# Kernel optimization log

Hardware: AMD Instinct MI355X
Metric: run time of the kernel (lower is better)

Reference implementation:

```python
import math
import jax, jax.numpy as jnp
import numpy as np

B, S, H, NH = 2, 2048, 1024, 16
HD = H // NH


def setup_inputs() -> dict:
    key = jax.random.key(0)
    k1, k2, k3 = jax.random.split(key, 3)
    scale = 1.0 / math.sqrt(H)
    return {
        "hidden_states": jax.random.normal(k1, (B, S, H), dtype=jnp.float32),
        "attention_mask": jnp.ones((B, 1, S, S), dtype=jnp.float32),
        "qkv_w": jax.random.normal(k2, (3 * H, H), dtype=jnp.float32) * scale,
        "qkv_b": jnp.zeros((3 * H,), dtype=jnp.float32),
        "dense_w": jax.random.normal(k3, (H, H), dtype=jnp.float32) * scale,
        "dense_b": jnp.zeros((H,), dtype=jnp.float32),
    }


def reference(hidden_states, attention_mask, qkv_w, qkv_b, dense_w, dense_b):
    # qkv projection: torch Linear y = x @ W^T + b
    mixed = hidden_states @ qkv_w.T + qkv_b            # [B,S,3H]
    mixed = mixed.reshape(B, S, NH, 3 * HD).transpose(0, 2, 1, 3)  # [B,NH,S,3HD]
    q, k, v = jnp.split(mixed, 3, axis=-1)             # each [B,NH,S,HD]
    scores = jnp.einsum("bhqd,bhkd->bhqk", q, k) / math.sqrt(HD)
    scores = scores * attention_mask - 10000.0 * (1.0 - attention_mask)
    probs = jax.nn.softmax(scores, axis=-1)            # dropout p=0 -> identity
    ctx = jnp.einsum("bhqk,bhkd->bhqd", probs, v)      # [B,NH,S,HD]
    ctx = ctx.transpose(0, 2, 1, 3).reshape(B, S, H)
    out = ctx @ dense_w.T + dense_b                    # output dropout p=0
    return out
```

## Files before the change

kernel.cpp:

```cpp
#include <hip/hip_runtime.h>
#include <hip/hip_bf16.h>
#include <stdint.h>

#define BB 2
#define SS 2048
#define HH 1024
#define NHH 16
#define HDD 64
#define MM (BB*SS)
#define N1 (3*HH)
#define NT (SS/64)
#define LOG2E 1.44269504f

using bf16 = __hip_bfloat16;
typedef __attribute__((ext_vector_type(8))) short bf16x8;
typedef __attribute__((ext_vector_type(4))) float f32x4;

__device__ inline unsigned short f2bfu(float f) {
  union { bf16 h; unsigned short u; } c;
  c.h = __float2bfloat16(f);
  return c.u;
}

__device__ inline unsigned int cvtpk(float lo, float hi) {
  unsigned int r;
  asm("v_cvt_pk_bf16_f32 %0, %1, %2" : "=v"(r) : "v"(lo), "v"(hi));
  return r;
}

__device__ inline void load_lds16(const void* g, void* l) {
  __builtin_amdgcn_global_load_lds(
      (const __attribute__((address_space(1))) void*)g,
      (__attribute__((address_space(3))) void*)l, 16, 0, 0);
}

__device__ inline f32x4 mfma16(bf16x8 a, bf16x8 b, f32x4 c) {
  return __builtin_amdgcn_mfma_f32_16x16x32_bf16(a, b, c, 0, 0, 0);
}

__global__ __launch_bounds__(256) void cvt_f32_bf16(const float* __restrict__ in,
                                                    unsigned short* __restrict__ out,
                                                    int n4) {
  int i = blockIdx.x * blockDim.x + threadIdx.x;
  int st = gridDim.x * blockDim.x;
  for (; i < n4; i += st) {
    float4 v = reinterpret_cast<const float4*>(in)[i];
    ushort4 o;
    o.x = f2bfu(v.x); o.y = f2bfu(v.y); o.z = f2bfu(v.z); o.w = f2bfu(v.w);
    reinterpret_cast<ushort4*>(out)[i] = o;
  }
}

__global__ __launch_bounds__(256) void mask_flags_kernel(const float* __restrict__ mask,
                                                         unsigned char* __restrict__ flags) {
  int t = blockIdx.x;
  int b = t >> 10, qt = (t >> 5) & 31, kt = t & 31;
  const float* mb = mask + ((size_t)b * SS + qt * 64) * SS + kt * 64;
  int row = threadIdx.x >> 2, c0 = (threadIdx.x & 3) * 16;
  int ok = 1;
#pragma unroll
  for (int j = 0; j < 4; ++j) {
    float4 v = *reinterpret_cast<const float4*>(mb + (size_t)row * SS + c0 + j * 4);
    ok &= (v.x == 1.f) & (v.y == 1.f) & (v.z == 1.f) & (v.w == 1.f);
  }
  ok = __all(ok);
  __shared__ int s[4];
  if ((threadIdx.x & 63) == 0) s[threadIdx.x >> 6] = ok;
  __syncthreads();
  if (threadIdx.x == 0) flags[t] = (unsigned char)(s[0] & s[1] & s[2] & s[3]);
}

__global__ __launch_bounds__(256) void vtrans_kernel(const unsigned short* __restrict__ mixed,
                                                     unsigned short* __restrict__ vT) {
  __shared__ unsigned short t[64 * 72];
  const int st = blockIdx.x, bh = blockIdx.y;
  const int b = bh >> 4, h = bh & 15;
  const int r = threadIdx.x >> 2, c0 = (threadIdx.x & 3) * 16;

  const unsigned short* src = mixed + ((size_t)(b * SS) + st * 64) * N1 + h * 192 + 128;
  union { bf16x8 v; unsigned short u[8]; } A, B;
  A.v = *reinterpret_cast<const bf16x8*>(src + (size_t)r * N1 + c0);
  B.v = *reinterpret_cast<const bf16x8*>(src + (size_t)r * N1 + c0 + 8);
#pragma unroll
  for (int j = 0; j < 8; ++j) t[(c0 + j) * 72 + r] = A.u[j];
#pragma unroll
  for (int j = 0; j < 8; ++j) t[(c0 + 8 + j) * 72 + r] = B.u[j];
  __syncthreads();

  unsigned short* dst = vT + ((size_t)bh * HDD + r) * SS + st * 64 + c0;
  bf16x8 o0 = *reinterpret_cast<const bf16x8*>(&t[r * 72 + c0]);
  bf16x8 o1 = *reinterpret_cast<const bf16x8*>(&t[r * 72 + c0 + 8]);
  *reinterpret_cast<bf16x8*>(dst) = o0;
  *reinterpret_cast<bf16x8*>(dst + 8) = o1;
}

template <bool OUT_BF16>
__global__ __launch_bounds__(256) void gemm_bt(const unsigned short* __restrict__ A,
                                               const unsigned short* __restrict__ Bt,
                                               const float* __restrict__ bias,
                                               void* __restrict__ Cv,
                                               int Ndim, int Kdim) {
  __shared__ __align__(16) unsigned short As[128 * 32];
  __shared__ __align__(16) unsigned short Bs[128 * 32];

  const int tid = threadIdx.x;
  const int wave = tid >> 6, lane = tid & 63;
  const int m0 = blockIdx.x * 128;
  const int n0 = blockIdx.y * 128;
  const int wm = (wave >> 1) * 64, wn = (wave & 1) * 64;
  const int lrow = lane & 15;
  const int lk8 = (lane >> 4) * 8;
  const int r4 = (lane >> 4) * 4;

  f32x4 acc[4][4];
  const f32x4 z = {0.f, 0.f, 0.f, 0.f};
  for (int i = 0; i < 4; ++i)
    for (int j = 0; j < 4; ++j) acc[i][j] = z;

  for (int k0 = 0; k0 < Kdim; k0 += 32) {
#pragma unroll
    for (int it = 0; it < 2; ++it) {
      int idx = it * 256 + tid;
      int row = idx >> 2, seg = idx & 3;
      load_lds16(A + (size_t)(m0 + row) * Kdim + k0 + seg * 8, &As[row * 32 + seg * 8]);
      load_lds16(Bt + (size_t)(n0 + row) * Kdim + k0 + seg * 8, &Bs[row * 32 + seg * 8]);
    }
    __syncthreads();

    bf16x8 af[4], bfr[4];
#pragma unroll
    for (int i = 0; i < 4; ++i)
      af[i] = *reinterpret_cast<const bf16x8*>(&As[(wm + i * 16 + lrow) * 32 + lk8]);
#pragma unroll
    for (int j = 0; j < 4; ++j)
      bfr[j] = *reinterpret_cast<const bf16x8*>(&Bs[(wn + j * 16 + lrow) * 32 + lk8]);
#pragma unroll
    for (int i = 0; i < 4; ++i)
#pragma unroll
      for (int j = 0; j < 4; ++j)
        acc[i][j] = mfma16(af[i], bfr[j], acc[i][j]);
    __syncthreads();
  }

#pragma unroll
  for (int i = 0; i < 4; ++i) {
#pragma unroll
    for (int j = 0; j < 4; ++j) {
      int col = n0 + wn + j * 16 + lrow;
      float bv = bias[col];
#pragma unroll
      for (int r = 0; r < 4; ++r) {
        int row = m0 + wm + i * 16 + r4 + r;
        float v = acc[i][j][r] + bv;
        if (OUT_BF16) {
          ((unsigned short*)Cv)[(size_t)row * Ndim + col] = f2bfu(v);
        } else {
          ((float*)Cv)[(size_t)row * Ndim + col] = v;
        }
      }
    }
  }
}

__global__ __launch_bounds__(256, 4) void attn_kernel(const unsigned short* __restrict__ mixed,
                                                      const unsigned short* __restrict__ vT,
                                                      const float* __restrict__ mask,
                                                      const unsigned char* __restrict__ flags,
                                                      unsigned short* __restrict__ ctx) {
  __shared__ __align__(16) unsigned short Ks[2][64 * 64];
  __shared__ __align__(16) unsigned short Vt[2][64 * 64];
  __shared__ __align__(16) unsigned short QP[64 * 64];

  const int tid = threadIdx.x, wave = tid >> 6, lane = tid & 63;
  const int ql = lane & 15;
  const int g = lane >> 4;
  const int q0 = blockIdx.x * 64;
  const int bh = blockIdx.y;
  const int b = bh / NHH, hh = bh % NHH;

  const unsigned short* qbase = mixed + (size_t)(b * SS) * N1 + hh * 192;
  const unsigned short* kbase = qbase + 64;
  const unsigned short* vtbase = vT + ((size_t)(b * NHH + hh) * HDD) * SS;
  const float* mbase = mask + (size_t)b * SS * SS;
  const unsigned char* fl = flags + ((size_t)b * 32 + blockIdx.x) * 32;

  const int srow = tid >> 3, sseg = tid & 7;
  const int swst = (sseg ^ (srow & 7)) << 3;

  load_lds16(qbase + (size_t)(q0 + srow) * N1 + swst, &QP[srow * 64 + sseg * 8]);
  load_lds16(qbase + (size_t)(q0 + 32 + srow) * N1 + swst, &QP[(32 + srow) * 64 + sseg * 8]);
  load_lds16(kbase + (size_t)srow * N1 + swst, &Ks[0][srow * 64 + sseg * 8]);
  load_lds16(kbase + (size_t)(32 + srow) * N1 + swst, &Ks[0][(32 + srow) * 64 + sseg * 8]);
  load_lds16(vtbase + (size_t)srow * SS + swst, &Vt[0][srow * 64 + sseg * 8]);
  load_lds16(vtbase + (size_t)(32 + srow) * SS + swst, &Vt[0][(32 + srow) * 64 + sseg * 8]);
  __syncthreads();

  const int qrow = wave * 16 + ql;
  const bf16x8 qf0 = *reinterpret_cast<const bf16x8*>(
      &QP[qrow * 64 + ((g ^ (qrow & 7)) << 3)]);
  const bf16x8 qf1 = *reinterpret_cast<const bf16x8*>(
      &QP[qrow * 64 + (((g + 4) ^ (qrow & 7)) << 3)]);
  __syncthreads();

  const int s0 = (g ^ (ql & 7)) << 3;
  const int s1 = ((g + 4) ^ (ql & 7)) << 3;
  const unsigned short* KrA = &Ks[0][ql * 64 + s0];
  const unsigned short* KrB = &Ks[0][ql * 64 + s1];
  const unsigned short* VrA = &Vt[0][ql * 64 + s0];
  const unsigned short* VrB = &Vt[0][ql * 64 + s1];
  unsigned short* Ps = &QP[wave * 1024];
  const int X = (ql & 7) << 3;
  unsigned short* Pw0 = &Ps[ql * 64 + ((4 * g) ^ X)];
  unsigned short* Pw1 = &Ps[ql * 64 + ((16 + 4 * g) ^ X)];
  unsigned short* Pw2 = &Ps[ql * 64 + ((32 + 4 * g) ^ X)];
  unsigned short* Pw3 = &Ps[ql * 64 + ((48 + 4 * g) ^ X)];
  const unsigned short* Pr0 = &Ps[ql * 64 + ((8 * g) ^ X)];
  const unsigned short* Pr1 = &Ps[ql * 64 + ((32 + 8 * g) ^ X)];

  const unsigned short* kpre = kbase + (size_t)(64 + srow) * N1 + swst;
  const unsigned short* vpre = vtbase + (size_t)srow * SS + 64 + swst;

  f32x4 oacc[4];
  const f32x4 z = {0.f, 0.f, 0.f, 0.f};
  for (int fd = 0; fd < 4; ++fd) oacc[fd] = z;
  float lsum = 0.f;
  const float C2 = 0.125f * LOG2E;

#define TILE_BODY(CUR_, KT_, HAVENEXT_)                                         \
  {                                                                             \
    const int kt_ = (KT_);                                                      \
    if (HAVENEXT_) {                                                            \
      load_lds16(kpre, &Ks[(CUR_)^1][srow * 64 + sseg * 8]);                    \
      load_lds16(kpre + 32 * N1, &Ks[(CUR_)^1][(32 + srow) * 64 + sseg * 8]);   \
      load_lds16(vpre, &Vt[(CUR_)^1][srow * 64 + sseg * 8]);                    \
      load_lds16(vpre + 32 * SS, &Vt[(CUR_)^1][(32 + srow) * 64 + sseg * 8]);   \
    }                                                                           \
    kpre += 64 * N1; vpre += 64;                                                \
    f32x4 sacc[4];                                                              \
    __builtin_amdgcn_s_setprio(1);                                              \
    _Pragma("unroll")                                                           \
    for (int n = 0; n < 4; ++n) {                                               \
      bf16x8 k0 = *reinterpret_cast<const bf16x8*>(KrA + (CUR_)*4096 + n*1024); \
      bf16x8 k1 = *reinterpret_cast<const bf16x8*>(KrB + (CUR_)*4096 + n*1024); \
      sacc[n] = mfma16(k0, qf0, z);                                             \
      sacc[n] = mfma16(k1, qf1, sacc[n]);                                       \
    }                                                                           \
    __builtin_amdgcn_s_setprio(0);                                              \
    const bool allones = fl[kt_] != 0;                                          \
    float pv[4][4];                                                             \
    if (allones) {                                                              \
      _Pragma("unroll")                                                         \
      for (int n = 0; n < 4; ++n)                                               \
        _Pragma("unroll")                                                       \
        for (int r = 0; r < 4; ++r)                                             \
          pv[n][r] = exp2f(sacc[n][r] * C2);                                    \
    } else {                                                                    \
      int qq = q0 + wave * 16 + ql;                                             \
      _Pragma("unroll")                                                         \
      for (int n = 0; n < 4; ++n)                                               \
        _Pragma("unroll")                                                       \
        for (int r = 0; r < 4; ++r) {                                           \
          int kk = kt_ * 64 + 16 * n + 4 * g + r;                               \
          float mv = mbase[(size_t)qq * SS + kk];                               \
          float s = sacc[n][r] * 0.125f;                                        \
          pv[n][r] = exp2f((s * mv - 10000.f * (1.f - mv)) * LOG2E);            \
        }                                                                       \
    }                                                                           \
    {                                                                           \
      float t00 = (pv[0][0] + pv[0][1]) + (pv[0][2] + pv[0][3]);                \
      float t01 = (pv[1][0] + pv[1][1]) + (pv[1][2] + pv[1][3]);                \
      float t10 = (pv[2][0] + pv[2][1]) + (pv[2][2] + pv[2][3]);                \
      float t11 = (pv[3][0] + pv[3][1]) + (pv[3][2] + pv[3][3]);                \
      lsum += (t00 + t01) + (t10 + t11);                                        \
    }                                                                           \
    { uint2 w; w.x = cvtpk(pv[0][0], pv[0][1]); w.y = cvtpk(pv[0][2], pv[0][3]);\
      *reinterpret_cast<uint2*>(Pw0) = w; }                                     \
    { uint2 w; w.x = cvtpk(pv[1][0], pv[1][1]); w.y = cvtpk(pv[1][2], pv[1][3]);\
      *reinterpret_cast<uint2*>(Pw1) = w; }                                     \
    { uint2 w; w.x = cvtpk(pv[2][0], pv[2][1]); w.y = cvtpk(pv[2][2], pv[2][3]);\
      *reinterpret_cast<uint2*>(Pw2) = w; }                                     \
    { uint2 w; w.x = cvtpk(pv[3][0], pv[3][1]); w.y = cvtpk(pv[3][2], pv[3][3]);\
      *reinterpret_cast<uint2*>(Pw3) = w; }                                     \
    bf16x8 pa0 = *reinterpret_cast<const bf16x8*>(Pr0);                         \
    bf16x8 pa1 = *reinterpret_cast<const bf16x8*>(Pr1);                         \
    __builtin_amdgcn_s_setprio(1);                                              \
    _Pragma("unroll")                                                           \
    for (int fd = 0; fd < 4; ++fd) {                                            \
      bf16x8 bv0 = *reinterpret_cast<const bf16x8*>(VrA + (CUR_)*4096 + fd*1024);\
      bf16x8 bv1 = *reinterpret_cast<const bf16x8*>(VrB + (CUR_)*4096 + fd*1024);\
      oacc[fd] = mfma16(pa0, bv0, oacc[fd]);                                    \
      oacc[fd] = mfma16(pa1, bv1, oacc[fd]);                                    \
    }                                                                           \
    __builtin_amdgcn_s_setprio(0);                                              \
    __syncthreads();                                                            \
  }

  for (int kt = 0; kt < NT; kt += 2) {
    TILE_BODY(0, kt, true)
    TILE_BODY(1, kt + 1, (kt + 2 < NT))
  }
#undef TILE_BODY

  float lrun = lsum;
  lrun += __shfl_xor(lrun, 16, 64);
  lrun += __shfl_xor(lrun, 32, 64);
  float invl = 1.f / lrun;
#pragma unroll
  for (int r = 0; r < 4; ++r) {
    float inv = __shfl(invl, g * 4 + r, 64);
    int qq = q0 + wave * 16 + g * 4 + r;
    unsigned short* cp = ctx + (size_t)(b * SS + qq) * HH + hh * HDD;
#pragma unroll
    for (int fd = 0; fd < 4; ++fd)
      cp[fd * 16 + ql] = f2bfu(oacc[fd][r] * inv);
  }
}

extern "C" void kernel_launch(void* const* d_in, const int* in_sizes, int n_in,
                              void* d_out, int out_size, void* d_ws, size_t ws_size,
                              hipStream_t stream) {
  const float* hs      = (const float*)d_in[0];
  const float* mask    = (const float*)d_in[1];
  const float* qkv_w   = (const float*)d_in[2];
  const float* qkv_b   = (const float*)d_in[3];
  const float* dense_w = (const float*)d_in[4];
  const float* dense_b = (const float*)d_in[5];
  float* out = (float*)d_out;

  char* ws = (char*)d_ws;
  unsigned short* hs_b     = (unsigned short*)(ws);
  unsigned short* qkvw_b   = (unsigned short*)(ws + 8388608);
  unsigned short* densew_b = (unsigned short*)(ws + 14680064);
  unsigned short* mixed_b  = (unsigned short*)(ws + 16777216);
  unsigned short* ctx_b    = (unsigned short*)(ws + 41943040);
  unsigned char*  flags    = (unsigned char*)(ws + 50331648);
  unsigned short* vT_b     = (unsigned short*)(ws + 50335744);

  cvt_f32_bf16<<<2048, 256, 0, stream>>>(hs, hs_b, (MM * HH) / 4);
  cvt_f32_bf16<<<2048, 256, 0, stream>>>(qkv_w, qkvw_b, (N1 * HH) / 4);
  cvt_f32_bf16<<<1024, 256, 0, stream>>>(dense_w, densew_b, (HH * HH) / 4);
  mask_flags_kernel<<<BB * 32 * 32, 256, 0, stream>>>(mask, flags);

  gemm_bt<true><<<dim3(MM / 128, N1 / 128), 256, 0, stream>>>(
      hs_b, qkvw_b, qkv_b, mixed_b, N1, HH);

  vtrans_kernel<<<dim3(SS / 64, BB * NHH), 256, 0, stream>>>(mixed_b, vT_b);

  attn_kernel<<<dim3(SS / 64, BB * NHH), 256, 0, stream>>>(
      mixed_b, vT_b, mask, flags, ctx_b);

  gemm_bt<false><<<dim3(MM / 128, HH / 128), 256, 0, stream>>>(
      ctx_b, densew_b, dense_b, out, HH, HH);
}
```

Before: 157.2 us.

## Load V tiles directly into registers instead of staging through LDS

V^T fragments for the PV MFMA are now loaded from global memory straight into per-lane registers, double-buffered across key tiles, and the LDS Vt buffers are removed. This is meant to cut LDS traffic and LDS footprint, which could allow more occupancy. In exchange each wave issues its own global loads for V, so V is fetched redundantly across the four waves, and register pressure rises by 16 bf16x8 vectors, which may reduce occupancy under the 256x4 launch bounds.

```diff
diff --git a/kernel.cpp b/kernel.cpp
--- a/kernel.cpp
+++ b/kernel.cpp
@@ -168,7 +168,6 @@
                                                       const unsigned char* __restrict__ flags,
                                                       unsigned short* __restrict__ ctx) {
   __shared__ __align__(16) unsigned short Ks[2][64 * 64];
-  __shared__ __align__(16) unsigned short Vt[2][64 * 64];
   __shared__ __align__(16) unsigned short QP[64 * 64];
 
   const int tid = threadIdx.x, wave = tid >> 6, lane = tid & 63;
@@ -191,8 +190,22 @@
   load_lds16(qbase + (size_t)(q0 + 32 + srow) * N1 + swst, &QP[(32 + srow) * 64 + sseg * 8]);
   load_lds16(kbase + (size_t)srow * N1 + swst, &Ks[0][srow * 64 + sseg * 8]);
   load_lds16(kbase + (size_t)(32 + srow) * N1 + swst, &Ks[0][(32 + srow) * 64 + sseg * 8]);
-  load_lds16(vtbase + (size_t)srow * SS + swst, &Vt[0][srow * 64 + sseg * 8]);
-  load_lds16(vtbase + (size_t)(32 + srow) * SS + swst, &Vt[0][(32 + srow) * 64 + sseg * 8]);
+
+  const unsigned short* vp0 = vtbase + (size_t)(0 * 16 + ql) * SS + g * 8;
+  const unsigned short* vp1 = vtbase + (size_t)(1 * 16 + ql) * SS + g * 8;
+  const unsigned short* vp2 = vtbase + (size_t)(2 * 16 + ql) * SS + g * 8;
+  const unsigned short* vp3 = vtbase + (size_t)(3 * 16 + ql) * SS + g * 8;
+
+  bf16x8 vrA[8], vrB[8];
+  vrA[0] = *reinterpret_cast<const bf16x8*>(vp0);
+  vrA[1] = *reinterpret_cast<const bf16x8*>(vp1);
+  vrA[2] = *reinterpret_cast<const bf16x8*>(vp2);
+  vrA[3] = *reinterpret_cast<const bf16x8*>(vp3);
+  vrA[4] = *reinterpret_cast<const bf16x8*>(vp0 + 32);
+  vrA[5] = *reinterpret_cast<const bf16x8*>(vp1 + 32);
+  vrA[6] = *reinterpret_cast<const bf16x8*>(vp2 + 32);
+  vrA[7] = *reinterpret_cast<const bf16x8*>(vp3 + 32);
+  vp0 += 64; vp1 += 64; vp2 += 64; vp3 += 64;
   __syncthreads();
 
   const int qrow = wave * 16 + ql;
@@ -206,8 +219,6 @@
   const int s1 = ((g + 4) ^ (ql & 7)) << 3;
   const unsigned short* KrA = &Ks[0][ql * 64 + s0];
   const unsigned short* KrB = &Ks[0][ql * 64 + s1];
-  const unsigned short* VrA = &Vt[0][ql * 64 + s0];
-  const unsigned short* VrB = &Vt[0][ql * 64 + s1];
   unsigned short* Ps = &QP[wave * 1024];
   const int X = (ql & 7) << 3;
   unsigned short* Pw0 = &Ps[ql * 64 + ((4 * g) ^ X)];
@@ -218,7 +229,6 @@
   const unsigned short* Pr1 = &Ps[ql * 64 + ((32 + 8 * g) ^ X)];
 
   const unsigned short* kpre = kbase + (size_t)(64 + srow) * N1 + swst;
-  const unsigned short* vpre = vtbase + (size_t)srow * SS + 64 + swst;
 
   f32x4 oacc[4];
   const f32x4 z = {0.f, 0.f, 0.f, 0.f};
@@ -226,16 +236,23 @@
   float lsum = 0.f;
   const float C2 = 0.125f * LOG2E;
 
-#define TILE_BODY(CUR_, KT_, HAVENEXT_)                                         \
+#define TILE_BODY(CUR_, KT_, HAVENEXT_, VCUR, VNXT)                             \
   {                                                                             \
     const int kt_ = (KT_);                                                      \
     if (HAVENEXT_) {                                                            \
       load_lds16(kpre, &Ks[(CUR_)^1][srow * 64 + sseg * 8]);                    \
       load_lds16(kpre + 32 * N1, &Ks[(CUR_)^1][(32 + srow) * 64 + sseg * 8]);   \
-      load_lds16(vpre, &Vt[(CUR_)^1][srow * 64 + sseg * 8]);                    \
-      load_lds16(vpre + 32 * SS, &Vt[(CUR_)^1][(32 + srow) * 64 + sseg * 8]);   \
-    }                                                                           \
-    kpre += 64 * N1; vpre += 64;                                                \
+      VNXT[0] = *reinterpret_cast<const bf16x8*>(vp0);                          \
+      VNXT[1] = *reinterpret_cast<const bf16x8*>(vp1);                          \
+      VNXT[2] = *reinterpret_cast<const bf16x8*>(vp2);                          \
+      VNXT[3] = *reinterpret_cast<const bf16x8*>(vp3);                          \
+      VNXT[4] = *reinterpret_cast<const bf16x8*>(vp0 + 32);                     \
+      VNXT[5] = *reinterpret_cast<const bf16x8*>(vp1 + 32);                     \
+      VNXT[6] = *reinterpret_cast<const bf16x8*>(vp2 + 32);                     \
+      VNXT[7] = *reinterpret_cast<const bf16x8*>(vp3 + 32);                     \
+    }                                                                           \
+    kpre += 64 * N1;                                                            \
+    vp0 += 64; vp1 += 64; vp2 += 64; vp3 += 64;                                 \
     f32x4 sacc[4];                                                              \
     __builtin_amdgcn_s_setprio(1);                                              \
     _Pragma("unroll")                                                           \
@@ -286,18 +303,16 @@
     __builtin_amdgcn_s_setprio(1);                                              \
     _Pragma("unroll")                                                           \
     for (int fd = 0; fd < 4; ++fd) {                                            \
-      bf16x8 bv0 = *reinterpret_cast<const bf16x8*>(VrA + (CUR_)*4096 + fd*1024);\
-      bf16x8 bv1 = *reinterpret_cast<const bf16x8*>(VrB + (CUR_)*4096 + fd*1024);\
-      oacc[fd] = mfma16(pa0, bv0, oacc[fd]);                                    \
-      oacc[fd] = mfma16(pa1, bv1, oacc[fd]);                                    \
+      oacc[fd] = mfma16(pa0, VCUR[fd], oacc[fd]);                               \
+      oacc[fd] = mfma16(pa1, VCUR[4 + fd], oacc[fd]);                           \
     }                                                                           \
     __builtin_amdgcn_s_setprio(0);                                              \
     __syncthreads();                                                            \
   }
 
   for (int kt = 0; kt < NT; kt += 2) {
-    TILE_BODY(0, kt, true)
-    TILE_BODY(1, kt + 1, (kt + 2 < NT))
+    TILE_BODY(0, kt, true, vrA, vrB)
+    TILE_BODY(1, kt + 1, (kt + 2 < NT), vrB, vrA)
   }
 #undef TILE_BODY
 
```

After: 317.1 us. 102% more time.
